# Performance work log

Measured on AMD Instinct MI355X. Metric: run time of the kernel, lower is better.

Reference implementation:

```python
import jax, jax.numpy as jnp
import numpy as np

B = 64        # number of graphs
NPG = 4096    # nodes per graph (equal-size segments, batch ids sorted)
H = 256       # hidden_dim
C0, C1 = 256, 64  # num_clusters


def setup_inputs() -> dict:
    key = jax.random.key(0)
    ks = jax.random.split(key, 8)
    N = B * NPG
    x = jax.random.normal(ks[0], (N, H), dtype=jnp.float32)
    edge_index = jax.random.randint(ks[1], (2, N), 0, N, dtype=jnp.int64)  # unused by forward
    batch = jnp.repeat(jnp.arange(B, dtype=jnp.int64), NPG)  # sorted, equal-size segments
    s = 1.0 / np.sqrt(H)
    W0 = jax.random.uniform(ks[2], (H, C0), jnp.float32, -s, s)
    b0 = jax.random.uniform(ks[3], (C0,), jnp.float32, -s, s)
    W1 = jax.random.uniform(ks[4], (H, C1), jnp.float32, -s, s)
    b1 = jax.random.uniform(ks[5], (C1,), jnp.float32, -s, s)
    sf = 1.0 / np.sqrt(C1 * H)
    Wf = jax.random.uniform(ks[6], (C1 * H, H), jnp.float32, -sf, sf)
    bf = jax.random.uniform(ks[7], (H,), jnp.float32, -sf, sf)
    return {"x": x, "edge_index": edge_index, "batch": batch,
            "W0": W0, "b0": b0, "W1": W1, "b1": b1, "Wf": Wf, "bf": bf}


def reference(x, edge_index, batch, W0, b0, W1, b1, Wf, bf):
    # Level 0: softmax cluster assignment + per-graph segmented matmul A^T @ F.
    # batch ids are sorted with equal-size segments, so the per-graph Python
    # loop of the original collapses to a reshape + batched einsum.
    A0 = jax.nn.softmax(x @ W0 + b0, axis=-1)                      # [N, C0]
    f0 = jnp.einsum('bnc,bnh->bch',
                    A0.reshape(B, NPG, C0),
                    x.reshape(B, NPG, H)).reshape(B * C0, H)        # [B*C0, H]
    # Level 1: same pattern on pooled cluster features (C0 'nodes' per graph).
    A1 = jax.nn.softmax(f0 @ W1 + b1, axis=-1)                     # [B*C0, C1]
    f1 = jnp.einsum('bnc,bnh->bch',
                    A1.reshape(B, C0, C1),
                    f0.reshape(B, C0, H)).reshape(B, C1 * H)        # [B, C1*H]
    # Final pool: Linear -> ReLU (Dropout is identity in eval mode).
    return jax.nn.relu(f1 @ Wf + bf)                               # [B, H]
```

## Files before the change

kernel.cpp:

```cpp
#include <hip/hip_runtime.h>
#include <stdint.h>

#define NG   64
#define NPG  4096
#define HD   256
#define NC0  256
#define NC1  64

typedef __attribute__((ext_vector_type(8))) short bfx8;
typedef __attribute__((ext_vector_type(4))) float fx4;

__device__ __forceinline__ unsigned short f2bf(float f) {
  union { float f; unsigned int u; } v; v.f = f;
  return (unsigned short)((v.u + 0x7FFFu + ((v.u >> 16) & 1u)) >> 16);
}
__device__ __forceinline__ unsigned int pack2(float a, float b) {
  return (unsigned int)f2bf(a) | ((unsigned int)f2bf(b) << 16);
}

#define ASYNC_COPY16(gptr, lptr) \
  __builtin_amdgcn_global_load_lds((const __attribute__((address_space(1))) unsigned int*)(gptr), \
                                   (__attribute__((address_space(3))) unsigned int*)(lptr), 16, 0, 0)

__global__ __launch_bounds__(256) void k_w0f(const float* __restrict__ W0,
                                             unsigned short* __restrict__ W0F) {
  int gid = blockIdx.x * 256 + threadIdx.x;
  int l15 = gid & 15;
  int q   = (gid >> 4) & 3;
  int ks  = (gid >> 6) & 1;
  int kc  = (gid >> 7) & 3;
  int cblk = gid >> 9;
  int c = cblk * 16 + l15;
  int kb = kc * 64 + ks * 32 + q * 8;
  unsigned int u[4];
  #pragma unroll
  for (int j = 0; j < 8; j += 2)
    u[j >> 1] = pack2(W0[(size_t)(kb + j) * 256 + c], W0[(size_t)(kb + j + 1) * 256 + c]);
  *(float4*)(W0F + (size_t)gid * 8) = *(float4*)u;
}

__global__ __launch_bounds__(256, 3) void k_assign0(
    const float* __restrict__ x, const unsigned short* __restrict__ W0F,
    const float* __restrict__ b0, unsigned short* __restrict__ A0T,
    unsigned short* __restrict__ xT, int g0) {
  __shared__ unsigned short lds_u[9216];
  __shared__ float red[64 * 4];

  int gl = blockIdx.x >> 6, nt = blockIdx.x & 63;
  int tid = threadIdx.x;
  int wn = tid >> 6, lane = tid & 63;
  int l15 = lane & 15, q = lane >> 4;

  fx4 acc[4][4];
  #pragma unroll
  for (int i = 0; i < 4; ++i)
    #pragma unroll
    for (int j = 0; j < 4; ++j) acc[i][j] = fx4{0.f, 0.f, 0.f, 0.f};

  const float* xbase = x + ((size_t)(g0 + gl) * NPG + (size_t)nt * 64) * HD;
  int snode = tid >> 2, sseg = (tid & 3) * 16;
  int sg0  = (tid & 3) * 2;
  int ssw  = (snode ^ (snode >> 4)) & 7;

  bfx8 bvc[4], bvn[4];
  #pragma unroll
  for (int ni = 0; ni < 4; ++ni)
    bvc[ni] = *(const bfx8*)(W0F + ((size_t)(((wn * 4 + ni) * 8 + 0) * 64 + lane)) * 8);

  {
    const float4* src = (const float4*)(xbase + (size_t)snode * HD + sseg);
    float4 v0 = src[0], v1 = src[1], v2 = src[2], v3 = src[3];
    float4 pv[2]; unsigned int* pu = (unsigned int*)pv;
    pu[0] = pack2(v0.x, v0.y); pu[1] = pack2(v0.z, v0.w);
    pu[2] = pack2(v1.x, v1.y); pu[3] = pack2(v1.z, v1.w);
    pu[4] = pack2(v2.x, v2.y); pu[5] = pack2(v2.z, v2.w);
    pu[6] = pack2(v3.x, v3.y); pu[7] = pack2(v3.z, v3.w);
    unsigned short* drow = &lds_u[snode << 6];
    *(float4*)(drow + (((sg0    ) ^ ssw) << 3)) = pv[0];
    *(float4*)(drow + (((sg0 + 1) ^ ssw) << 3)) = pv[1];
  }
  __syncthreads();

  for (int kc = 0; kc < 4; ++kc) {
    const unsigned short* xb = &lds_u[(kc & 1) * 4096];
    float4 v0, v1, v2, v3;
    if (kc < 3) {
      const float4* src = (const float4*)(xbase + (size_t)snode * HD + (kc + 1) * 64 + sseg);
      v0 = src[0]; v1 = src[1]; v2 = src[2]; v3 = src[3];
    }
    #pragma unroll
    for (int ks = 0; ks < 2; ++ks) {
      int g8 = kc * 2 + ks;
      if (g8 < 7) {
        #pragma unroll
        for (int ni = 0; ni < 4; ++ni)
          bvn[ni] = *(const bfx8*)(W0F + ((size_t)(((wn * 4 + ni) * 8 + g8 + 1) * 64 + lane)) * 8);
      }
      bfx8 af[4];
      #pragma unroll
      for (int mi = 0; mi < 4; ++mi) {
        int row = mi * 16 + l15;
        int slot = (ks * 4 + q) ^ ((row ^ (row >> 4)) & 7);
        af[mi] = *(const bfx8*)&xb[(row << 6) + (slot << 3)];
      }
      #pragma unroll
      for (int ni = 0; ni < 4; ++ni)
        #pragma unroll
        for (int mi = 0; mi < 4; ++mi)
          acc[mi][ni] = __builtin_amdgcn_mfma_f32_16x16x32_bf16(af[mi], bvc[ni], acc[mi][ni], 0, 0, 0);
      if (g8 < 7) {
        #pragma unroll
        for (int ni = 0; ni < 4; ++ni) bvc[ni] = bvn[ni];
      }
    }
    {
      int hl = tid >> 2, s4 = tid & 3, sgn = s4 * 16;
      int g = hl >> 3, off = hl & 7;
      unsigned int u[8];
      #pragma unroll
      for (int i = 0; i < 16; i += 2) {
        int n0 = sgn + i, n1 = n0 + 1;
        unsigned short a = xb[(n0 << 6) + ((g ^ ((n0 ^ (n0 >> 4)) & 7)) << 3) + off];
        unsigned short b = xb[(n1 << 6) + ((g ^ ((n1 ^ (n1 >> 4)) & 7)) << 3) + off];
        u[i >> 1] = (unsigned int)a | ((unsigned int)b << 16);
      }
      float4* dst = (float4*)(xT + ((size_t)(gl * 64 + nt) * HD + kc * 64 + hl) * 64 + sgn);
      dst[0] = *(float4*)&u[0];
      dst[1] = *(float4*)&u[4];
    }
    if (kc < 3) {
      float4 pv[2]; unsigned int* pu = (unsigned int*)pv;
      pu[0] = pack2(v0.x, v0.y); pu[1] = pack2(v0.z, v0.w);
      pu[2] = pack2(v1.x, v1.y); pu[3] = pack2(v1.z, v1.w);
      pu[4] = pack2(v2.x, v2.y); pu[5] = pack2(v2.z, v2.w);
      pu[6] = pack2(v3.x, v3.y); pu[7] = pack2(v3.z, v3.w);
      unsigned short* drow = &lds_u[(((kc & 1) ^ 1) * 4096) + (snode << 6)];
      *(float4*)(drow + (((sg0    ) ^ ssw) << 3)) = pv[0];
      *(float4*)(drow + (((sg0 + 1) ^ ssw) << 3)) = pv[1];
    }
    __syncthreads();
  }

  float bv4[4];
  #pragma unroll
  for (int ni = 0; ni < 4; ++ni) bv4[ni] = b0[wn * 64 + ni * 16 + l15];
  #pragma unroll
  for (int mi = 0; mi < 4; ++mi)
    #pragma unroll
    for (int ni = 0; ni < 4; ++ni)
      #pragma unroll
      for (int r = 0; r < 4; ++r) acc[mi][ni][r] += bv4[ni];

  float mrow[4][4];
  #pragma unroll
  for (int mi = 0; mi < 4; ++mi)
    #pragma unroll
    for (int r = 0; r < 4; ++r) {
      float m = fmaxf(fmaxf(acc[mi][0][r], acc[mi][1][r]), fmaxf(acc[mi][2][r], acc[mi][3][r]));
      #pragma unroll
      for (int off = 1; off < 16; off <<= 1) m = fmaxf(m, __shfl_xor(m, off));
      mrow[mi][r] = m;
    }
  if (l15 == 0) {
    #pragma unroll
    for (int mi = 0; mi < 4; ++mi)
      #pragma unroll
      for (int r = 0; r < 4; ++r)
        red[(mi * 16 + q * 4 + r) * 4 + wn] = mrow[mi][r];
  }
  __syncthreads();
  #pragma unroll
  for (int mi = 0; mi < 4; ++mi)
    #pragma unroll
    for (int r = 0; r < 4; ++r) {
      float4 rv = *(const float4*)&red[(mi * 16 + q * 4 + r) * 4];
      mrow[mi][r] = fmaxf(fmaxf(rv.x, rv.y), fmaxf(rv.z, rv.w));
    }
  __syncthreads();
  float srow[4][4];
  #pragma unroll
  for (int mi = 0; mi < 4; ++mi)
    #pragma unroll
    for (int r = 0; r < 4; ++r) {
      float s = 0.f;
      #pragma unroll
      for (int ni = 0; ni < 4; ++ni) {
        float e = __expf(acc[mi][ni][r] - mrow[mi][r]);
        acc[mi][ni][r] = e; s += e;
      }
      #pragma unroll
      for (int off = 1; off < 16; off <<= 1) s += __shfl_xor(s, off);
      srow[mi][r] = s;
    }
  if (l15 == 0) {
    #pragma unroll
    for (int mi = 0; mi < 4; ++mi)
      #pragma unroll
      for (int r = 0; r < 4; ++r)
        red[(mi * 16 + q * 4 + r) * 4 + wn] = srow[mi][r];
  }
  __syncthreads();
  #pragma unroll
  for (int mi = 0; mi < 4; ++mi)
    #pragma unroll
    for (int r = 0; r < 4; ++r) {
      float4 rv = *(const float4*)&red[(mi * 16 + q * 4 + r) * 4];
      float inv = 1.f / (rv.x + rv.y + rv.z + rv.w);
      #pragma unroll
      for (int ni = 0; ni < 4; ++ni) acc[mi][ni][r] *= inv;
    }
  __syncthreads();

  unsigned short* at = lds_u;
  unsigned short* A0Tg = A0T + (size_t)(gl * 64 + nt) * NC0 * 64;
  #pragma unroll
  for (int p = 0; p < 2; ++p) {
    if ((wn >> 1) == p) {
      int cb = (wn & 1) * 64;
      #pragma unroll
      for (int mi = 0; mi < 4; ++mi) {
        int ncol = mi * 16 + q * 4;
        #pragma unroll
        for (int ni = 0; ni < 4; ++ni) {
          int cl = cb + ni * 16 + l15;
          uint2 w;
          w.x = pack2(acc[mi][ni][0], acc[mi][ni][1]);
          w.y = pack2(acc[mi][ni][2], acc[mi][ni][3]);
          *(uint2*)(at + cl * 72 + ncol) = w;
        }
      }
    }
    __syncthreads();
    {
      int row = tid >> 1, sg2 = (tid & 1) * 32;
      const float4* s4p = (const float4*)(at + row * 72 + sg2);
      float4 a = s4p[0], b = s4p[1], c = s4p[2], d = s4p[3];
      float4* d4 = (float4*)(A0Tg + (size_t)(p * 128 + row) * 64 + sg2);
      d4[0] = a; d4[1] = b; d4[2] = c; d4[3] = d;
    }
    __syncthreads();
  }
}

__global__ __launch_bounds__(512, 2) void k_pool0(
    const unsigned short* __restrict__ A0T, const unsigned short* __restrict__ xT,
    float* __restrict__ f0, int g0) {
  __shared__ unsigned short a_s[2][128 * 64];
  __shared__ unsigned short b_s[2][128 * 64];
  int bid = blockIdx.x;
  int gl, mt, nt;
  if (gridDim.x == 256) {
    int xcd = bid & 7, s = bid >> 3;
    gl = xcd + 8 * (s >> 2);
    int j = s & 3;
    mt = j >> 1; nt = j & 1;
  } else {
    nt = bid & 1; mt = (bid >> 1) & 1; gl = bid >> 2;
  }

  int tid = threadIdx.x;
  int wave = tid >> 6, lane = tid & 63;
  int wm = wave >> 2, wn = wave & 3;
  int l15 = lane & 15, q = lane >> 4;

  const unsigned short* abase = A0T + (size_t)gl * 64 * NC0 * 64 + (size_t)mt * 128 * 64;
  const unsigned short* bbase = xT  + (size_t)gl * 64 * HD  * 64 + (size_t)nt * 128 * 64;

  fx4 acc[4][2];
  #pragma unroll
  for (int i = 0; i < 4; ++i)
    #pragma unroll
    for (int j = 0; j < 2; ++j) acc[i][j] = fx4{0.f, 0.f, 0.f, 0.f};

  int srow = lane >> 3;
  int sg   = (lane & 7) ^ srow;
  size_t soff = (size_t)srow * 64 + (size_t)sg * 8;

  #pragma unroll
  for (int c = 0; c < 2; ++c) {
    size_t co = (size_t)c * 16384;
    #pragma unroll
    for (int i = 0; i < 2; ++i) {
      int r0 = wave * 16 + i * 8;
      ASYNC_COPY16(abase + co + (size_t)r0 * 64 + soff, &a_s[c][r0 * 64]);
      ASYNC_COPY16(bbase + co + (size_t)r0 * 64 + soff, &b_s[c][r0 * 64]);
    }
  }

  for (int t = 0; t < NPG / 64; ++t) {
    int buf = t & 1;
    if (t < NPG / 64 - 1) asm volatile("s_waitcnt vmcnt(4)" ::: "memory");
    else                  asm volatile("s_waitcnt vmcnt(0)" ::: "memory");
    __builtin_amdgcn_s_barrier();

    bfx8 af[2][4], bf[2][2];
    #pragma unroll
    for (int ks = 0; ks < 2; ++ks) {
      int gx = ((ks * 4 + q) ^ (l15 & 7)) << 3;
      #pragma unroll
      for (int mi = 0; mi < 4; ++mi)
        af[ks][mi] = *(const bfx8*)&a_s[buf][(wm * 64 + mi * 16 + l15) * 64 + gx];
      #pragma unroll
      for (int ni = 0; ni < 2; ++ni)
        bf[ks][ni] = *(const bfx8*)&b_s[buf][(wn * 32 + ni * 16 + l15) * 64 + gx];
    }
    asm volatile("s_waitcnt lgkmcnt(0)" ::: "memory");
    __builtin_amdgcn_s_barrier();

    if (t + 2 < NPG / 64) {
      size_t co = (size_t)(t + 2) * 16384;
      #pragma unroll
      for (int i = 0; i < 2; ++i) {
        int r0 = wave * 16 + i * 8;
        ASYNC_COPY16(abase + co + (size_t)r0 * 64 + soff, &a_s[buf][r0 * 64]);
        ASYNC_COPY16(bbase + co + (size_t)r0 * 64 + soff, &b_s[buf][r0 * 64]);
      }
    }
    #pragma unroll
    for (int ks = 0; ks < 2; ++ks)
      #pragma unroll
      for (int ni = 0; ni < 2; ++ni)
        #pragma unroll
        for (int mi = 0; mi < 4; ++mi)
          acc[mi][ni] = __builtin_amdgcn_mfma_f32_16x16x32_bf16(af[ks][mi], bf[ks][ni], acc[mi][ni], 0, 0, 0);
  }

  float* dst = f0 + ((size_t)(g0 + gl) * NC0 + (size_t)mt * 128) * HD + (size_t)nt * 128;
  #pragma unroll
  for (int mi = 0; mi < 4; ++mi)
    #pragma unroll
    for (int ni = 0; ni < 2; ++ni) {
      int c = wm * 64 + mi * 16 + q * 4;
      int h = wn * 32 + ni * 16 + l15;
      #pragma unroll
      for (int r = 0; r < 4; ++r)
        dst[(size_t)(c + r) * HD + h] = acc[mi][ni][r];
    }
}

__global__ __launch_bounds__(256) void k_assign1(
    const float* __restrict__ f0, const float* __restrict__ W1,
    const float* __restrict__ b1, float* __restrict__ A1) {
  __shared__ float w1s[256 * 64];
  int tid = threadIdx.x;
  #pragma unroll
  for (int i = 0; i < 16; ++i) {
    int off = i * 1024 + tid * 4;
    *(float4*)(w1s + off) = *(const float4*)(W1 + off);
  }
  __syncthreads();
  int lane = tid & 63;
  int rbase = blockIdx.x * 32 + (tid >> 6) * 8;
  float bias = b1[lane];
  for (int rr = 0; rr < 8; ++rr) {
    int row = rbase + rr;
    const float* fr = f0 + (size_t)row * 256;
    float acc = bias;
    for (int k = 0; k < 256; k += 4) {
      float4 fv = *(const float4*)(fr + k);
      acc += fv.x * w1s[(k    ) * 64 + lane];
      acc += fv.y * w1s[(k + 1) * 64 + lane];
      acc += fv.z * w1s[(k + 2) * 64 + lane];
      acc += fv.w * w1s[(k + 3) * 64 + lane];
    }
    float m = acc;
    #pragma unroll
    for (int off = 1; off < 64; off <<= 1) m = fmaxf(m, __shfl_xor(m, off));
    float e = __expf(acc - m);
    float s = e;
    #pragma unroll
    for (int off = 1; off < 64; off <<= 1) s += __shfl_xor(s, off);
    A1[(size_t)row * 64 + lane] = e / s;
  }
}

__global__ __launch_bounds__(256) void k_pool1(
    const float* __restrict__ A1, const float* __restrict__ f0, float* __restrict__ f1) {
  int b = blockIdx.x >> 2, cg = blockIdx.x & 3;
  int h = threadIdx.x;
  const float* a1p = A1 + (size_t)b * NC0 * NC1 + cg * 16;
  const float* f0p = f0 + (size_t)b * NC0 * HD + h;
  float acc[16];
  #pragma unroll
  for (int j = 0; j < 16; ++j) acc[j] = 0.f;
  for (int c0 = 0; c0 < 256; ++c0) {
    float fv = f0p[(size_t)c0 * 256];
    #pragma unroll
    for (int j = 0; j < 16; ++j) acc[j] += a1p[c0 * 64 + j] * fv;
  }
  float* d = f1 + (size_t)b * 16384 + (size_t)(cg * 16) * 256 + h;
  #pragma unroll
  for (int j = 0; j < 16; ++j) d[(size_t)j * 256] = acc[j];
}

__global__ __launch_bounds__(512) void k_final_partial(
    const float* __restrict__ f1, const float* __restrict__ Wf, float* __restrict__ ot) {
  __shared__ float f1s[64 * 256];
  int ht = blockIdx.x & 1;
  int ks = blockIdx.x >> 1;
  int tid = threadIdx.x;
  {
    int b = tid >> 3, c0 = (tid & 7) * 4;
    const float* s = f1 + (size_t)b * 16384 + (size_t)ks * 256 + c0;
    float* d = f1s + b * 256 + c0;
    #pragma unroll
    for (int i = 0; i < 8; ++i) *(float4*)(d + i * 32) = *(const float4*)(s + i * 32);
  }
  __syncthreads();
  int h = ht * 128 + (tid & 127);
  int b0 = (tid >> 7) * 16;
  const float* wp = Wf + (size_t)ks * 256 * 256 + h;
  float acc[16];
  #pragma unroll
  for (int j = 0; j < 16; ++j) acc[j] = 0.f;
  for (int k = 0; k < 256; k += 4) {
    float w0 = wp[(size_t)(k    ) * 256];
    float w1 = wp[(size_t)(k + 1) * 256];
    float w2 = wp[(size_t)(k + 2) * 256];
    float w3 = wp[(size_t)(k + 3) * 256];
    #pragma unroll
    for (int j = 0; j < 16; ++j) {
      float4 fv = *(const float4*)(f1s + (b0 + j) * 256 + k);
      acc[j] += fv.x * w0 + fv.y * w1 + fv.z * w2 + fv.w * w3;
    }
  }
  #pragma unroll
  for (int j = 0; j < 16; ++j) atomicAdd(&ot[(b0 + j) * 256 + h], acc[j]);
}

__global__ __launch_bounds__(256) void k_final_out(
    const float* __restrict__ ot, const float* __restrict__ bfv, float* __restrict__ out) {
  int i = blockIdx.x * 256 + threadIdx.x;
  float v = ot[i] + bfv[i & 255];
  out[i] = v > 0.f ? v : 0.f;
}

extern "C" void kernel_launch(void* const* d_in, const int* in_sizes, int n_in,
                              void* d_out, int out_size, void* d_ws, size_t ws_size,
                              hipStream_t stream) {
  const float* x   = (const float*)d_in[0];
  const float* W0  = (const float*)d_in[3];
  const float* b0  = (const float*)d_in[4];
  const float* W1  = (const float*)d_in[5];
  const float* b1  = (const float*)d_in[6];
  const float* Wf  = (const float*)d_in[7];
  const float* bfv = (const float*)d_in[8];
  float* out = (float*)d_out;
  char* ws = (char*)d_ws;

  float* f0  = (float*)ws;
  float* ot  = (float*)(ws + ((size_t)32 << 20));
  unsigned short* W0F = (unsigned short*)(ws + ((size_t)32 << 20) + 65536);
  size_t chunk_off = ((size_t)32 << 20) + 65536 + 131072;
  size_t per_graph = (size_t)4 * HD * NPG;
  size_t avail = ws_size > chunk_off ? ws_size - chunk_off : 0;
  int G = (int)(avail / per_graph);
  if (G > 64) G = 64;
  if (G < 1) G = 1;
  unsigned short* xT  = (unsigned short*)(ws + chunk_off);
  unsigned short* A0T = xT + (size_t)G * HD * NPG;
  float* f1 = (float*)xT;
  float* A1 = (float*)A0T;

  hipMemsetAsync(ot, 0, 65536, stream);
  k_w0f<<<32, 256, 0, stream>>>(W0, W0F);

  for (int g0 = 0; g0 < NG; g0 += G) {
    int gc = (NG - g0 < G) ? (NG - g0) : G;
    k_assign0<<<gc * 64, 256, 0, stream>>>(x, W0F, b0, A0T, xT, g0);
    k_pool0<<<gc * 4, 512, 0, stream>>>(A0T, xT, f0, g0);
  }
  k_assign1<<<512, 256, 0, stream>>>(f0, W1, b1, A1);
  k_pool1<<<256, 256, 0, stream>>>(A1, f0, f1);
  k_final_partial<<<128, 512, 0, stream>>>(f1, Wf, ot);
  k_final_out<<<64, 256, 0, stream>>>(ot, bfv, out);
}
```

Baseline: 654.9 us.

## Split pool0 reduction over nodes, parallelize pool1 and final GEMV across more blocks

k_pool0 now splits the 4096-node reduction into two halves handled by separate blocks, writing two partial f0 buffers that a new k_f0sum kernel adds together. The chunk size is capped at 32 graphs so the grid stays at 256 blocks while running twice per forward. k_pool1 uses 1024 threads and splits the c0 loop four ways with a shared-memory reduction. k_final_partial doubles its grid by splitting the batch in two. These raise parallelism in kernels that were underfilled, at the cost of an extra launch, more f0 traffic and an extra chunk iteration. The second partial buffer sits at offset NG*NC0*HD*4 bytes, which ends exactly where ot begins, so the workspace layout only just fits.

Result: no change. 644.9 us (-1.5%).

```diff
diff --git a/kernel.cpp b/kernel.cpp
--- a/kernel.cpp
+++ b/kernel.cpp
@@ -6,6 +6,7 @@
 #define HD   256
 #define NC0  256
 #define NC1  64
+#define KSPLIT 2
 
 typedef __attribute__((ext_vector_type(8))) short bfx8;
 typedef __attribute__((ext_vector_type(4))) float fx4;
@@ -244,18 +245,18 @@
 
 __global__ __launch_bounds__(512, 2) void k_pool0(
     const unsigned short* __restrict__ A0T, const unsigned short* __restrict__ xT,
-    float* __restrict__ f0, int g0) {
+    float* __restrict__ f0p, int g0) {
   __shared__ unsigned short a_s[2][128 * 64];
   __shared__ unsigned short b_s[2][128 * 64];
   int bid = blockIdx.x;
-  int gl, mt, nt;
+  int gl, mt, nt, kidx;
   if (gridDim.x == 256) {
     int xcd = bid & 7, s = bid >> 3;
-    gl = xcd + 8 * (s >> 2);
-    int j = s & 3;
-    mt = j >> 1; nt = j & 1;
+    int p = xcd + 8 * (s >> 2);
+    gl = p & 31; kidx = p >> 5;
+    int j = s & 3; mt = j >> 1; nt = j & 1;
   } else {
-    nt = bid & 1; mt = (bid >> 1) & 1; gl = bid >> 2;
+    nt = bid & 1; mt = (bid >> 1) & 1; kidx = (bid >> 2) & 1; gl = bid >> 3;
   }
 
   int tid = threadIdx.x;
@@ -263,8 +264,9 @@
   int wm = wave >> 2, wn = wave & 3;
   int l15 = lane & 15, q = lane >> 4;
 
-  const unsigned short* abase = A0T + (size_t)gl * 64 * NC0 * 64 + (size_t)mt * 128 * 64;
-  const unsigned short* bbase = xT  + (size_t)gl * 64 * HD  * 64 + (size_t)nt * 128 * 64;
+  const int TPK = (NPG / 64) / KSPLIT;
+  const unsigned short* abase = A0T + (size_t)gl * 64 * NC0 * 64 + (size_t)kidx * TPK * 16384 + (size_t)mt * 128 * 64;
+  const unsigned short* bbase = xT  + (size_t)gl * 64 * HD  * 64 + (size_t)kidx * TPK * 16384 + (size_t)nt * 128 * 64;
 
   fx4 acc[4][2];
   #pragma unroll
@@ -287,10 +289,10 @@
     }
   }
 
-  for (int t = 0; t < NPG / 64; ++t) {
+  for (int t = 0; t < TPK; ++t) {
     int buf = t & 1;
-    if (t < NPG / 64 - 1) asm volatile("s_waitcnt vmcnt(4)" ::: "memory");
-    else                  asm volatile("s_waitcnt vmcnt(0)" ::: "memory");
+    if (t < TPK - 1) asm volatile("s_waitcnt vmcnt(4)" ::: "memory");
+    else             asm volatile("s_waitcnt vmcnt(0)" ::: "memory");
     __builtin_amdgcn_s_barrier();
 
     bfx8 af[2][4], bf[2][2];
@@ -307,7 +309,7 @@
     asm volatile("s_waitcnt lgkmcnt(0)" ::: "memory");
     __builtin_amdgcn_s_barrier();
 
-    if (t + 2 < NPG / 64) {
+    if (t + 2 < TPK) {
       size_t co = (size_t)(t + 2) * 16384;
       #pragma unroll
       for (int i = 0; i < 2; ++i) {
@@ -325,7 +327,8 @@
           acc[mi][ni] = __builtin_amdgcn_mfma_f32_16x16x32_bf16(af[ks][mi], bf[ks][ni], acc[mi][ni], 0, 0, 0);
   }
 
-  float* dst = f0 + ((size_t)(g0 + gl) * NC0 + (size_t)mt * 128) * HD + (size_t)nt * 128;
+  float* dst = f0p + (size_t)kidx * NG * NC0 * HD
+             + ((size_t)(g0 + gl) * NC0 + (size_t)mt * 128) * HD + (size_t)nt * 128;
   #pragma unroll
   for (int mi = 0; mi < 4; ++mi)
     #pragma unroll
@@ -336,6 +339,14 @@
       for (int r = 0; r < 4; ++r)
         dst[(size_t)(c + r) * HD + h] = acc[mi][ni][r];
     }
+}
+
+__global__ __launch_bounds__(256) void k_f0sum(float* __restrict__ f0) {
+  size_t i = ((size_t)blockIdx.x * 256 + threadIdx.x) * 4;
+  float4 a = *(const float4*)(f0 + i);
+  float4 b = *(const float4*)(f0 + (size_t)NG * NC0 * HD + i);
+  a.x += b.x; a.y += b.y; a.z += b.z; a.w += b.w;
+  *(float4*)(f0 + i) = a;
 }
 
 __global__ __launch_bounds__(256) void k_assign1(
@@ -374,58 +385,76 @@
   }
 }
 
-__global__ __launch_bounds__(256) void k_pool1(
+__global__ __launch_bounds__(1024) void k_pool1(
     const float* __restrict__ A1, const float* __restrict__ f0, float* __restrict__ f1) {
+  __shared__ float part[3 * 256 * 16];
   int b = blockIdx.x >> 2, cg = blockIdx.x & 3;
-  int h = threadIdx.x;
+  int tid = threadIdx.x;
+  int c0g = tid >> 8;
+  int h = tid & 255;
   const float* a1p = A1 + (size_t)b * NC0 * NC1 + cg * 16;
   const float* f0p = f0 + (size_t)b * NC0 * HD + h;
   float acc[16];
   #pragma unroll
   for (int j = 0; j < 16; ++j) acc[j] = 0.f;
-  for (int c0 = 0; c0 < 256; ++c0) {
+  for (int c0 = c0g * 64; c0 < c0g * 64 + 64; ++c0) {
     float fv = f0p[(size_t)c0 * 256];
     #pragma unroll
     for (int j = 0; j < 16; ++j) acc[j] += a1p[c0 * 64 + j] * fv;
   }
-  float* d = f1 + (size_t)b * 16384 + (size_t)(cg * 16) * 256 + h;
-  #pragma unroll
-  for (int j = 0; j < 16; ++j) d[(size_t)j * 256] = acc[j];
+  if (c0g > 0) {
+    float* d = &part[((c0g - 1) * 256 + h) * 16];
+    #pragma unroll
+    for (int j = 0; j < 16; ++j) d[j] = acc[j];
+  }
+  __syncthreads();
+  if (c0g == 0) {
+    #pragma unroll
+    for (int g = 0; g < 3; ++g) {
+      const float* s = &part[(g * 256 + h) * 16];
+      #pragma unroll
+      for (int j = 0; j < 16; ++j) acc[j] += s[j];
+    }
+    float* d = f1 + (size_t)b * 16384 + (size_t)(cg * 16) * 256 + h;
+    #pragma unroll
+    for (int j = 0; j < 16; ++j) d[(size_t)j * 256] = acc[j];
+  }
 }
 
 __global__ __launch_bounds__(512) void k_final_partial(
     const float* __restrict__ f1, const float* __restrict__ Wf, float* __restrict__ ot) {
-  __shared__ float f1s[64 * 256];
-  int ht = blockIdx.x & 1;
-  int ks = blockIdx.x >> 1;
+  __shared__ float f1s[32 * 256];
+  int ks = blockIdx.x >> 2;
+  int ht = (blockIdx.x >> 1) & 1;
+  int bh = blockIdx.x & 1;
   int tid = threadIdx.x;
-  {
-    int b = tid >> 3, c0 = (tid & 7) * 4;
-    const float* s = f1 + (size_t)b * 16384 + (size_t)ks * 256 + c0;
-    float* d = f1s + b * 256 + c0;
-    #pragma unroll
-    for (int i = 0; i < 8; ++i) *(float4*)(d + i * 32) = *(const float4*)(s + i * 32);
+  #pragma unroll
+  for (int i = 0; i < 4; ++i) {
+    int idx = i * 512 + tid;
+    int bb = idx >> 6, c4 = idx & 63;
+    *(float4*)(f1s + bb * 256 + c4 * 4) =
+        *(const float4*)(f1 + (size_t)(bh * 32 + bb) * 16384 + (size_t)ks * 256 + c4 * 4);
   }
   __syncthreads();
   int h = ht * 128 + (tid & 127);
-  int b0 = (tid >> 7) * 16;
+  int b0 = (tid >> 7) * 8;
   const float* wp = Wf + (size_t)ks * 256 * 256 + h;
-  float acc[16];
-  #pragma unroll
-  for (int j = 0; j < 16; ++j) acc[j] = 0.f;
+  float acc[8];
+  #pragma unroll
+  for (int j = 0; j < 8; ++j) acc[j] = 0.f;
   for (int k = 0; k < 256; k += 4) {
     float w0 = wp[(size_t)(k    ) * 256];
     float w1 = wp[(size_t)(k + 1) * 256];
     float w2 = wp[(size_t)(k + 2) * 256];
     float w3 = wp[(size_t)(k + 3) * 256];
     #pragma unroll
-    for (int j = 0; j < 16; ++j) {
+    for (int j = 0; j < 8; ++j) {
       float4 fv = *(const float4*)(f1s + (b0 + j) * 256 + k);
       acc[j] += fv.x * w0 + fv.y * w1 + fv.z * w2 + fv.w * w3;
     }
   }
   #pragma unroll
-  for (int j = 0; j < 16; ++j) atomicAdd(&ot[(b0 + j) * 256 + h], acc[j]);
+  for (int j = 0; j < 8; ++j) atomicAdd(&ot[(bh * 32 + b0 + j) * 256 + h], acc[j]);
 }
 
 __global__ __launch_bounds__(256) void k_final_out(
@@ -448,14 +477,15 @@
   float* out = (float*)d_out;
   char* ws = (char*)d_ws;
 
-  float* f0  = (float*)ws;
+  float* f0p = (float*)ws;
+  float* f0  = f0p;
   float* ot  = (float*)(ws + ((size_t)32 << 20));
   unsigned short* W0F = (unsigned short*)(ws + ((size_t)32 << 20) + 65536);
   size_t chunk_off = ((size_t)32 << 20) + 65536 + 131072;
   size_t per_graph = (size_t)4 * HD * NPG;
   size_t avail = ws_size > chunk_off ? ws_size - chunk_off : 0;
   int G = (int)(avail / per_graph);
-  if (G > 64) G = 64;
+  if (G > 32) G = 32;
   if (G < 1) G = 1;
   unsigned short* xT  = (unsigned short*)(ws + chunk_off);
   unsigned short* A0T = xT + (size_t)G * HD * NPG;
@@ -468,10 +498,11 @@
   for (int g0 = 0; g0 < NG; g0 += G) {
     int gc = (NG - g0 < G) ? (NG - g0) : G;
     k_assign0<<<gc * 64, 256, 0, stream>>>(x, W0F, b0, A0T, xT, g0);
-    k_pool0<<<gc * 4, 512, 0, stream>>>(A0T, xT, f0, g0);
-  }
+    k_pool0<<<gc * 4 * KSPLIT, 512, 0, stream>>>(A0T, xT, f0p, g0);
+  }
+  k_f0sum<<<4096, 256, 0, stream>>>(f0);
   k_assign1<<<512, 256, 0, stream>>>(f0, W1, b1, A1);
-  k_pool1<<<256, 256, 0, stream>>>(A1, f0, f1);
-  k_final_partial<<<128, 512, 0, stream>>>(f1, Wf, ot);
+  k_pool1<<<256, 1024, 0, stream>>>(A1, f0, f1);
+  k_final_partial<<<256, 512, 0, stream>>>(f1, Wf, ot);
   k_final_out<<<64, 256, 0, stream>>>(ot, bfv, out);
 }
```
